# Optimization experiments

Hardware: AMD Instinct MI355X
Metric: run time of the kernel (lower is better)

The kernel has to match this reference:

```python
import jax, jax.numpy as jnp
import numpy as np

B, S, D, H, M = 4, 4096, 768, 12, 256
Dh = D // H
EPS_KERNEL = 1e-4
LN_EPS = 1e-5


def setup_inputs() -> dict:
    key = jax.random.key(0)
    ks = jax.random.split(key, 18)
    w = lambda k, sh: jax.random.normal(k, sh, jnp.float32) * 0.02
    return {
        "x": jax.random.normal(ks[0], (B, S, D), jnp.float32),
        # FAVOR+ random projection (performer uses orthogonal gaussian; gaussian here, same math)
        "proj": jax.random.normal(ks[1], (M, Dh), jnp.float32),
        "wq": w(ks[2], (D, D)), "bq": jnp.zeros((D,), jnp.float32),
        "wk": w(ks[3], (D, D)), "bk": jnp.zeros((D,), jnp.float32),
        "wv": w(ks[4], (D, D)), "bv": jnp.zeros((D,), jnp.float32),
        "wo": w(ks[5], (D, D)), "bo": jnp.zeros((D,), jnp.float32),
        "ln1_g": jnp.ones((D,), jnp.float32), "ln1_b": jnp.zeros((D,), jnp.float32),
        "ln2_g": jnp.ones((D,), jnp.float32), "ln2_b": jnp.zeros((D,), jnp.float32),
        "w1": w(ks[6], (4 * D, D)), "b1": jnp.zeros((4 * D,), jnp.float32),
        "w2": w(ks[7], (D, 4 * D)), "b2": jnp.zeros((D,), jnp.float32),
    }


def layernorm(x, g, b):
    mu = x.mean(-1, keepdims=True)
    var = ((x - mu) ** 2).mean(-1, keepdims=True)
    return (x - mu) / jnp.sqrt(var + LN_EPS) * g + b


def softmax_features(data, proj, is_query):
    # FAVOR+ positive softmax kernel features (performer-pytorch softmax_kernel)
    norm = data.shape[-1] ** -0.25
    ratio = proj.shape[0] ** -0.5
    dd = jnp.einsum('bhnd,md->bhnm', data * norm, proj)       # [B,H,S,M]
    diag = (data ** 2).sum(-1, keepdims=True) * 0.5 * norm * norm
    if is_query:
        mx = jnp.max(dd, axis=-1, keepdims=True)
    else:
        mx = jnp.max(dd)
    return ratio * (jnp.exp(dd - diag - mx) + EPS_KERNEL)


def performer_block(x, proj, wq, bq, wk, bk, wv, bv, wo, bo,
                    ln1_g, ln1_b, ln2_g, ln2_b, w1, b1, w2, b2):
    h = layernorm(x, ln1_g, ln1_b)
    split = lambda t: t.reshape(B, S, H, Dh).transpose(0, 2, 1, 3)  # [B,H,S,Dh]
    q = split(h @ wq.T + bq)
    k = split(h @ wk.T + bk)
    v = split(h @ wv.T + bv)

    qp = softmax_features(q, proj, True)    # [B,H,S,M]
    kp = softmax_features(k, proj, False)   # [B,H,S,M]

    # non-causal linear attention
    k_sum = kp.sum(axis=2)                                   # [B,H,M]
    d_inv = 1.0 / jnp.einsum('bhnm,bhm->bhn', qp, k_sum)     # [B,H,S]
    ctx = jnp.einsum('bhnm,bhnd->bhmd', kp, v)               # [B,H,M,Dh]
    attn = jnp.einsum('bhnm,bhmd,bhn->bhnd', qp, ctx, d_inv) # [B,H,S,Dh]
    attn = attn.transpose(0, 2, 1, 3).reshape(B, S, D)
    x = x + attn @ wo.T + bo

    h2 = layernorm(x, ln2_g, ln2_b)
    h2 = jax.nn.gelu(h2 @ w1.T + b1, approximate=False)
    x = x + h2 @ w2.T + b2
    return x


def reference(x, proj, wq, bq, wk, bk, wv, bv, wo, bo,
              ln1_g, ln1_b, ln2_g, ln2_b, w1, b1, w2, b2):
    return performer_block(x, proj, wq, bq, wk, bk, wv, bv, wo, bo,
                           ln1_g, ln1_b, ln2_g, ln2_b, w1, b1, w2, b2)
```

## Files before the change

### kernel.cpp

```cpp
#include <hip/hip_runtime.h>
#include <math.h>

typedef __attribute__((ext_vector_type(8))) short bf16x8;
typedef __attribute__((ext_vector_type(4))) float f32x4;

__device__ __forceinline__ float b2f(unsigned short u) {
    return __uint_as_float(((unsigned)u) << 16);
}
__device__ __forceinline__ unsigned short f2b(float f) {
    unsigned u = __float_as_uint(f);
    u += 0x7FFF + ((u >> 16) & 1);
    return (unsigned short)(u >> 16);
}
__device__ __forceinline__ void up2(unsigned u, float& a, float& b) {
    a = __uint_as_float(u << 16);
    b = __uint_as_float(u & 0xffff0000u);
}
__device__ __forceinline__ float gelu_exact(float v) {
    return 0.5f * v * (1.0f + erff(v * 0.70710678118654752f));
}
__device__ __forceinline__ void atomicMaxFloat(float* addr, float val) {
    unsigned* ua = (unsigned*)addr;
    unsigned old = *ua;
    while (true) {
        float of = __uint_as_float(old);
        if (of >= val) break;
        unsigned assumed = old;
        old = atomicCAS(ua, assumed, __float_as_uint(val));
        if (old == assumed) break;
    }
}
__device__ __forceinline__ void gl_lds16(const unsigned short* g, unsigned short* lds) {
    __builtin_amdgcn_global_load_lds((const __attribute__((address_space(1))) unsigned int*)g,
                                     (__attribute__((address_space(3))) unsigned int*)lds, 16, 0, 0);
}

__global__ __launch_bounds__(256)
void cvt_qkvp(const float* __restrict__ wq, const float* __restrict__ wk, const float* __restrict__ wv,
              const float* __restrict__ prj, unsigned short* __restrict__ wdst,
              unsigned short* __restrict__ pdst, float* __restrict__ ksum, float* __restrict__ kmax) {
    if (blockIdx.x < 48) {
        ksum[blockIdx.x * 256 + threadIdx.x] = 0.0f;
        if (blockIdx.x == 0 && threadIdx.x == 0) *kmax = -3.0e38f;
    }
    int i4 = (blockIdx.x * 256 + threadIdx.x) * 4;
    const float* s; unsigned short* d; int off;
    if (i4 < 1769472) { s = (i4 < 589824) ? wq : (i4 < 1179648 ? wk : wv);
        off = (i4 < 589824) ? i4 : (i4 < 1179648 ? i4 - 589824 : i4 - 1179648);
        d = wdst + i4; }
    else { s = prj; off = i4 - 1769472; d = pdst + off; }
    float4 v = *(const float4*)&s[off];
    ushort4 o; o.x = f2b(v.x); o.y = f2b(v.y); o.z = f2b(v.z); o.w = f2b(v.w);
    *(ushort4*)d = o;
}
__global__ __launch_bounds__(256)
void cvt_ow12(const float* __restrict__ wo, const float* __restrict__ w1, const float* __restrict__ w2,
              unsigned short* __restrict__ dst) {
    int i4 = (blockIdx.x * 256 + threadIdx.x) * 4;
    const float* s; int off;
    if (i4 < 589824) { s = wo; off = i4; }
    else if (i4 < 2949120) { s = w1; off = i4 - 589824; }
    else { s = w2; off = i4 - 2949120; }
    float4 v = *(const float4*)&s[off];
    ushort4 o; o.x = f2b(v.x); o.y = f2b(v.y); o.z = f2b(v.z); o.w = f2b(v.w);
    *(ushort4*)&dst[i4] = o;
}

template <bool IN_F32>
__global__ __launch_bounds__(256)
void ln_kernel(const void* __restrict__ Xv, const float* __restrict__ G,
               const float* __restrict__ Bb, unsigned short* __restrict__ OUT) {
    int row = blockIdx.x, t = threadIdx.x, wave = t >> 6, lane = t & 63;
    __shared__ float red[4];
    float x0, x1, x2;
    if constexpr (IN_F32) {
        const float* xr = (const float*)Xv + (size_t)row * 768;
        x0 = xr[t]; x1 = xr[t + 256]; x2 = xr[t + 512];
    } else {
        const unsigned short* xr = (const unsigned short*)Xv + (size_t)row * 768;
        x0 = b2f(xr[t]); x1 = b2f(xr[t + 256]); x2 = b2f(xr[t + 512]);
    }
    float s = x0 + x1 + x2;
#pragma unroll
    for (int d = 32; d; d >>= 1) s += __shfl_xor(s, d, 64);
    if (lane == 0) red[wave] = s;
    __syncthreads();
    float mean = (red[0] + red[1] + red[2] + red[3]) * (1.0f / 768.0f);
    __syncthreads();
    float d0 = x0 - mean, d1 = x1 - mean, d2 = x2 - mean;
    float s2 = d0 * d0 + d1 * d1 + d2 * d2;
#pragma unroll
    for (int d = 32; d; d >>= 1) s2 += __shfl_xor(s2, d, 64);
    if (lane == 0) red[wave] = s2;
    __syncthreads();
    float var = (red[0] + red[1] + red[2] + red[3]) * (1.0f / 768.0f);
    float inv = rsqrtf(var + 1e-5f);
    size_t base = (size_t)row * 768;
    OUT[base + t]       = f2b(d0 * inv * G[t]       + Bb[t]);
    OUT[base + t + 256] = f2b(d1 * inv * G[t + 256] + Bb[t + 256]);
    OUT[base + t + 512] = f2b(d2 * inv * G[t + 512] + Bb[t + 512]);
}

template <int EPI, bool R_F32, bool C_F32>
__global__ __launch_bounds__(512, 2)
void gemm_bt_256(const unsigned short* __restrict__ A, const unsigned short* __restrict__ Bm,
                 const float* __restrict__ bias, const void* __restrict__ R,
                 void* __restrict__ C, int N, int K, float alpha) {
    __shared__ unsigned short sA[2][256 * 64];
    __shared__ unsigned short sB[2][256 * 64];
    const int t = threadIdx.x;
    const int wave = t >> 6, lane = t & 63, quad = lane >> 4, l16 = lane & 15;
    const int nwg = gridDim.x * gridDim.y;
    int flat = blockIdx.y * gridDim.x + blockIdx.x;
    int q = nwg >> 3, r = nwg & 7;
    int xcd = flat & 7, idx = flat >> 3;
    int swz = (xcd < r ? xcd * (q + 1) : r * (q + 1) + (xcd - r) * q) + idx;
    const int m0 = (swz / gridDim.x) * 256;
    const int n0 = (swz % gridDim.x) * 256;
    const int wm = (wave >> 2) * 128, wn = (wave & 3) * 64;
    const int srow = t >> 3;
    const int scol = ((t & 7) ^ (srow & 7)) << 3;
    const unsigned short* gA = &A[(size_t)(m0 + srow) * K + scol];
    const unsigned short* gB = &Bm[(size_t)(n0 + srow) * K + scol];
    const size_t rstep = (size_t)64 * K;
    unsigned short* ldA0 = &sA[0][wave * 512];
    unsigned short* ldB0 = &sB[0][wave * 512];
    unsigned short* ldA1 = &sA[1][wave * 512];
    unsigned short* ldB1 = &sB[1][wave * 512];
    const int k0off = ((quad ^ (l16 & 7)) & 7) << 3;
    const int k1off = (((4 | quad) ^ (l16 & 7)) & 7) << 3;
    f32x4 acc[8][4] = {};
    const int nt = K >> 6;
#pragma unroll
    for (int u = 0; u < 4; ++u) {
        gl_lds16(gA + u * rstep, ldA0 + u * 4096);
        gl_lds16(gB + u * rstep, ldB0 + u * 4096);
    }
    __syncthreads();
    int cur = 0;
    for (int it = 0; it < nt; ++it) {
        if (it + 1 < nt) {
            const size_t kt = (size_t)(it + 1) << 6;
            unsigned short* dA = cur ? ldA0 : ldA1;
            unsigned short* dB = cur ? ldB0 : ldB1;
#pragma unroll
            for (int u = 0; u < 4; ++u) {
                gl_lds16(gA + u * rstep + kt, dA + u * 4096);
                gl_lds16(gB + u * rstep + kt, dB + u * 4096);
            }
        }
        const unsigned short* bufA = cur ? &sA[1][0] : &sA[0][0];
        const unsigned short* bufB = cur ? &sB[1][0] : &sB[0][0];
#pragma unroll
        for (int ks = 0; ks < 2; ++ks) {
            const int koff = ks ? k1off : k0off;
            bf16x8 bfr[4];
#pragma unroll
            for (int j = 0; j < 4; ++j)
                bfr[j] = *(const bf16x8*)&bufB[(wn + j * 16 + l16) * 64 + koff];
#pragma unroll
            for (int i = 0; i < 8; ++i) {
                bf16x8 af = *(const bf16x8*)&bufA[(wm + i * 16 + l16) * 64 + koff];
#pragma unroll
                for (int j = 0; j < 4; ++j)
                    acc[i][j] = __builtin_amdgcn_mfma_f32_16x16x32_bf16(af, bfr[j], acc[i][j], 0, 0, 0);
            }
        }
        __syncthreads();
        cur ^= 1;
    }
    if constexpr (EPI == 3) {
#pragma unroll
        for (int i = 0; i < 8; ++i) {
            int rowb = m0 + wm + i * 16 + quad * 4;
            int b_ = rowb >> 12, sbase = rowb & 4095;
#pragma unroll
            for (int j = 0; j < 4; ++j) {
                int col = n0 + wn + j * 16 + l16;
                float bs = bias[col];
                ushort4 o;
                o.x = f2b(acc[i][j][0] + bs);
                o.y = f2b(acc[i][j][1] + bs);
                o.z = f2b(acc[i][j][2] + bs);
                o.w = f2b(acc[i][j][3] + bs);
                size_t dst = (((size_t)b_ * 12 + (col >> 6)) * 64 + (col & 63)) * 4096 + sbase;
                *(ushort4*)&((unsigned short*)C)[dst] = o;
            }
        }
        return;
    }
#pragma unroll
    for (int i = 0; i < 8; ++i) {
        int rowb = m0 + wm + i * 16 + quad * 4;
#pragma unroll
        for (int j = 0; j < 4; ++j) {
            int col = n0 + wn + j * 16 + l16;
            float bs = bias[col];
#pragma unroll
            for (int r4 = 0; r4 < 4; ++r4) {
                size_t idx = (size_t)(rowb + r4) * N + col;
                float v = acc[i][j][r4] + bs;
                if constexpr (EPI == 0) v *= alpha;
                if constexpr (EPI == 1) {
                    if constexpr (R_F32) v += ((const float*)R)[idx];
                    else                 v += b2f(((const unsigned short*)R)[idx]);
                }
                if constexpr (EPI == 2) v = gelu_exact(v);
                if constexpr (C_F32) ((float*)C)[idx] = v;
                else                 ((unsigned short*)C)[idx] = f2b(v);
            }
        }
    }
}

__global__ __launch_bounds__(512, 2)
void gemm_qkv(const unsigned short* __restrict__ A, const unsigned short* __restrict__ Bm,
              const float* __restrict__ BQ, const float* __restrict__ BK,
              const float* __restrict__ BV, unsigned short* __restrict__ Cq,
              unsigned short* __restrict__ Ck, unsigned short* __restrict__ VT, float alpha) {
    const int K = 768;
    __shared__ unsigned short sA[2][256 * 64];
    __shared__ unsigned short sB[2][256 * 64];
    const int t = threadIdx.x;
    const int wave = t >> 6, lane = t & 63, quad = lane >> 4, l16 = lane & 15;
    const int nwg = gridDim.x * gridDim.y;
    int flat = blockIdx.y * gridDim.x + blockIdx.x;
    int q = nwg >> 3, r = nwg & 7;
    int xcd = flat & 7, idx = flat >> 3;
    int swz = (xcd < r ? xcd * (q + 1) : r * (q + 1) + (xcd - r) * q) + idx;
    const int m0 = (swz / gridDim.x) * 256;
    const int n0 = (swz % gridDim.x) * 256;
    const int wm = (wave >> 2) * 128, wn = (wave & 3) * 64;
    const int srow = t >> 3;
    const int scol = ((t & 7) ^ (srow & 7)) << 3;
    const unsigned short* gA = &A[(size_t)(m0 + srow) * K + scol];
    const unsigned short* gB = &Bm[(size_t)(n0 + srow) * K + scol];
    const size_t rstep = (size_t)64 * K;
    unsigned short* ldA0 = &sA[0][wave * 512];
    unsigned short* ldB0 = &sB[0][wave * 512];
    unsigned short* ldA1 = &sA[1][wave * 512];
    unsigned short* ldB1 = &sB[1][wave * 512];
    const int k0off = ((quad ^ (l16 & 7)) & 7) << 3;
    const int k1off = (((4 | quad) ^ (l16 & 7)) & 7) << 3;
    f32x4 acc[8][4] = {};
    const int nt = K >> 6;
#pragma unroll
    for (int u = 0; u < 4; ++u) {
        gl_lds16(gA + u * rstep, ldA0 + u * 4096);
        gl_lds16(gB + u * rstep, ldB0 + u * 4096);
    }
    __syncthreads();
    int cur = 0;
    for (int it = 0; it < nt; ++it) {
        if (it + 1 < nt) {
            const size_t kt = (size_t)(it + 1) << 6;
            unsigned short* dA = cur ? ldA0 : ldA1;
            unsigned short* dB = cur ? ldB0 : ldB1;
#pragma unroll
            for (int u = 0; u < 4; ++u) {
                gl_lds16(gA + u * rstep + kt, dA + u * 4096);
                gl_lds16(gB + u * rstep + kt, dB + u * 4096);
            }
        }
        const unsigned short* bufA = cur ? &sA[1][0] : &sA[0][0];
        const unsigned short* bufB = cur ? &sB[1][0] : &sB[0][0];
#pragma unroll
        for (int ks = 0; ks < 2; ++ks) {
            const int koff = ks ? k1off : k0off;
            bf16x8 bfr[4];
#pragma unroll
            for (int j = 0; j < 4; ++j)
                bfr[j] = *(const bf16x8*)&bufB[(wn + j * 16 + l16) * 64 + koff];
#pragma unroll
            for (int i = 0; i < 8; ++i) {
                bf16x8 af = *(const bf16x8*)&bufA[(wm + i * 16 + l16) * 64 + koff];
#pragma unroll
                for (int j = 0; j < 4; ++j)
                    acc[i][j] = __builtin_amdgcn_mfma_f32_16x16x32_bf16(af, bfr[j], acc[i][j], 0, 0, 0);
            }
        }
        __syncthreads();
        cur ^= 1;
    }
    const int seg = n0 / 768;
    const int nbase = n0 - seg * 768;
    const float* bias = (seg == 0) ? BQ : (seg == 1 ? BK : BV);
    if (seg == 2) {
#pragma unroll
        for (int i = 0; i < 8; ++i) {
            int rowb = m0 + wm + i * 16 + quad * 4;
            int b_ = rowb >> 12, sbase = rowb & 4095;
#pragma unroll
            for (int j = 0; j < 4; ++j) {
                int col = nbase + wn + j * 16 + l16;
                float bs = bias[col];
                ushort4 o;
                o.x = f2b(acc[i][j][0] + bs);
                o.y = f2b(acc[i][j][1] + bs);
                o.z = f2b(acc[i][j][2] + bs);
                o.w = f2b(acc[i][j][3] + bs);
                size_t dst = (((size_t)b_ * 12 + (col >> 6)) * 64 + (col & 63)) * 4096 + sbase;
                *(ushort4*)&VT[dst] = o;
            }
        }
    } else {
        unsigned short* Cn = (seg == 0) ? Cq : Ck;
#pragma unroll
        for (int i = 0; i < 8; ++i) {
            int rowb = m0 + wm + i * 16 + quad * 4;
#pragma unroll
            for (int j = 0; j < 4; ++j) {
                int col = nbase + wn + j * 16 + l16;
                float bs = bias[col];
#pragma unroll
                for (int r4 = 0; r4 < 4; ++r4) {
                    size_t idxo = (size_t)(rowb + r4) * 768 + col;
                    Cn[idxo] = f2b((acc[i][j][r4] + bs) * alpha);
                }
            }
        }
    }
}

template <int MODE>
__global__ __launch_bounds__(256)
void feat_kernel(const unsigned short* __restrict__ Q, const unsigned short* __restrict__ P,
                 unsigned short* __restrict__ OUTP, float* __restrict__ kmaxp,
                 float* __restrict__ ksump) {
    __shared__ unsigned short sQ[64 * 64];
    __shared__ unsigned short sP[256 * 64];
    __shared__ float sDiag[64];
    __shared__ float sRed[4];
    int t = threadIdx.x, wave = t >> 6, lane = t & 63, quad = lane >> 4, l16 = lane & 15;
    int bh = blockIdx.y, bq = bh / 12, hh = bh % 12;
    int s0 = blockIdx.x * 64;
    size_t rowbase = (size_t)bq * 4096 + s0;
#pragma unroll
    for (int u = 0; u < 2; ++u) {
        int L = u * 256 + t, row = L >> 3, c8 = (L & 7) * 8;
        *(uint4*)&sQ[row * 64 + c8] = *(const uint4*)&Q[(rowbase + row) * 768 + hh * 64 + c8];
    }
#pragma unroll
    for (int u = 0; u < 8; ++u) {
        int L = u * 256 + t, row = L >> 3, c8 = (L & 7) * 8;
        *(uint4*)&sP[row * 64 + c8] = *(const uint4*)&P[(size_t)row * 64 + c8];
    }
    __syncthreads();
    if (MODE != 1 && t < 64) {
        float d = 0.0f;
        for (int c = 0; c < 64; ++c) { float f = b2f(sQ[t * 64 + c]); d += f * f; }
        sDiag[t] = 0.5f * d;
    }
    f32x4 acc[4][4] = {};
#pragma unroll
    for (int ks = 0; ks < 2; ++ks) {
        bf16x8 af[4], bfr[4];
#pragma unroll
        for (int i = 0; i < 4; ++i) af[i] = *(const bf16x8*)&sQ[(i * 16 + l16) * 64 + ks * 32 + quad * 8];
#pragma unroll
        for (int j = 0; j < 4; ++j) bfr[j] = *(const bf16x8*)&sP[(wave * 64 + j * 16 + l16) * 64 + ks * 32 + quad * 8];
#pragma unroll
        for (int i = 0; i < 4; ++i)
#pragma unroll
            for (int j = 0; j < 4; ++j)
                acc[i][j] = __builtin_amdgcn_mfma_f32_16x16x32_bf16(af[i], bfr[j], acc[i][j], 0, 0, 0);
    }
    if constexpr (MODE == 1) {
        float m = -3.0e38f;
#pragma unroll
        for (int i = 0; i < 4; ++i)
#pragma unroll
            for (int j = 0; j < 4; ++j)
#pragma unroll
                for (int r = 0; r < 4; ++r) m = fmaxf(m, acc[i][j][r]);
#pragma unroll
        for (int d = 1; d < 64; d <<= 1) m = fmaxf(m, __shfl_xor(m, d, 64));
        if (lane == 0) sRed[wave] = m;
        __syncthreads();
        if (t == 0) atomicMaxFloat(kmaxp, fmaxf(fmaxf(sRed[0], sRed[1]), fmaxf(sRed[2], sRed[3])));
        return;
    } else {
        __syncthreads();
        float mx_k = *kmaxp;
        float csum[4] = {0.0f, 0.0f, 0.0f, 0.0f};
#pragma unroll
        for (int i = 0; i < 4; ++i)
#pragma unroll
            for (int j = 0; j < 4; ++j) {
                int col = wave * 64 + j * 16 + l16;
                ushort4 o;
#pragma unroll
                for (int r = 0; r < 4; ++r) {
                    int row = i * 16 + quad * 4 + r;
                    float v = 0.0625f * (expf(acc[i][j][r] - sDiag[row] - mx_k) + 1e-4f);
                    csum[j] += v;
                    (&o.x)[r] = f2b(v);
                }
                *(ushort4*)&OUTP[((size_t)bh * 256 + col) * 4096 + s0 + i * 16 + quad * 4] = o;
            }
#pragma unroll
        for (int j = 0; j < 4; ++j) {
            csum[j] += __shfl_xor(csum[j], 16, 64);
            csum[j] += __shfl_xor(csum[j], 32, 64);
        }
        if (quad == 0)
#pragma unroll
            for (int j = 0; j < 4; ++j)
                atomicAdd(&ksump[bh * 256 + wave * 64 + j * 16 + l16], csum[j]);
    }
}

__global__ __launch_bounds__(256)
void ctx_gemm(const unsigned short* __restrict__ KPT, const unsigned short* __restrict__ VT,
              float* __restrict__ part) {
    __shared__ unsigned short sV[2][64 * 32];
    __shared__ unsigned short sK[2][128 * 32];
    const int t = threadIdx.x;
    const int wave = t >> 6, lane = t & 63, quad = lane >> 4, l16 = lane & 15;
    const int bh = blockIdx.y;
    const int sc = blockIdx.x >> 1, mh = blockIdx.x & 1;
    const int m0 = mh * 128;
    const int k0 = sc * 512;
    const int srow = t >> 2;
    const int scol = ((t & 3) ^ (srow & 3)) << 3;
    const unsigned short* gv  = &VT [((size_t)bh * 64 + srow) * 4096 + k0 + scol];
    const unsigned short* gk0 = &KPT[((size_t)bh * 256 + m0 + srow) * 4096 + k0 + scol];
    const unsigned short* gk1 = &KPT[((size_t)bh * 256 + m0 + 64 + srow) * 4096 + k0 + scol];
    const int ldsoff = wave * 512;
    const int sw = ((quad ^ l16) & 3) << 3;
    f32x4 acc[4][2] = {};
    gl_lds16(gv,  &sV[0][ldsoff]);
    gl_lds16(gk0, &sK[0][ldsoff]);
    gl_lds16(gk1, &sK[0][2048 + ldsoff]);
    __syncthreads();
    int cur = 0;
    for (int it = 0; it < 16; ++it) {
        if (it + 1 < 16) {
            const int kt = (it + 1) << 5;
            gl_lds16(gv + kt,  &sV[cur ^ 1][ldsoff]);
            gl_lds16(gk0 + kt, &sK[cur ^ 1][ldsoff]);
            gl_lds16(gk1 + kt, &sK[cur ^ 1][2048 + ldsoff]);
        }
        bf16x8 af[4], bfr[2];
#pragma unroll
        for (int i = 0; i < 4; ++i) af[i] = *(const bf16x8*)&sV[cur][(i * 16 + l16) * 32 + sw];
#pragma unroll
        for (int j = 0; j < 2; ++j) bfr[j] = *(const bf16x8*)&sK[cur][(wave * 32 + j * 16 + l16) * 32 + sw];
#pragma unroll
        for (int i = 0; i < 4; ++i)
#pragma unroll
            for (int j = 0; j < 2; ++j)
                acc[i][j] = __builtin_amdgcn_mfma_f32_16x16x32_bf16(af[i], bfr[j], acc[i][j], 0, 0, 0);
        __syncthreads();
        cur ^= 1;
    }
    float* base = part + ((size_t)(sc * 48 + bh) * 64) * 256;
#pragma unroll
    for (int i = 0; i < 4; ++i)
#pragma unroll
        for (int r = 0; r < 4; ++r) {
            int d = i * 16 + quad * 4 + r;
#pragma unroll
            for (int j = 0; j < 2; ++j) {
                int m = m0 + wave * 32 + j * 16 + l16;
                base[(size_t)d * 256 + m] = acc[i][j][r];
            }
        }
}

__global__ __launch_bounds__(256)
void ctx_reduce(const float* __restrict__ part, unsigned short* __restrict__ ctxb) {
    size_t i = (size_t)blockIdx.x * 256 + threadIdx.x;
    float s = 0.0f;
#pragma unroll
    for (int c = 0; c < 8; ++c) s += part[(size_t)c * 786432 + i];
    ctxb[i] = f2b(s);
}

__global__ __launch_bounds__(256)
void feat_attn(const unsigned short* __restrict__ Q, const unsigned short* __restrict__ P,
               const unsigned short* __restrict__ CTX, const float* __restrict__ ksump,
               unsigned short* __restrict__ ATT) {
    __shared__ unsigned short sQ[64 * 64];
    __shared__ unsigned short sPQ[256 * 64];
    __shared__ unsigned short sCtx[64 * 256];
    __shared__ float sDiag[64];
    __shared__ float sRed[256];
    __shared__ float sWred[256];
    __shared__ float sKs[256];
    __shared__ float sDinv[64];
    int t = threadIdx.x, wave = t >> 6, lane = t & 63, quad = lane >> 4, l16 = lane & 15;
    int bh = blockIdx.y, bq = bh / 12, hh = bh % 12;
    int s0 = blockIdx.x * 64;
    size_t rowbase = (size_t)bq * 4096 + s0;
#pragma unroll
    for (int u = 0; u < 2; ++u) {
        int L = u * 256 + t, row = L >> 3, c8 = (L & 7) * 8;
        *(uint4*)&sQ[row * 64 + c8] = *(const uint4*)&Q[(rowbase + row) * 768 + hh * 64 + c8];
    }
#pragma unroll
    for (int u = 0; u < 8; ++u) {
        int L = u * 256 + t, row = L >> 3, c8 = (L & 7) * 8;
        *(uint4*)&sPQ[row * 64 + c8] = *(const uint4*)&P[(size_t)row * 64 + c8];
    }
#pragma unroll
    for (int u = 0; u < 8; ++u) {
        int L = u * 256 + t, d = L >> 5, m8 = L & 31;
        int m8s = (m8 & 28) | ((m8 ^ d) & 3);
        *(uint4*)&sCtx[d * 256 + m8s * 8] = *(const uint4*)&CTX[(size_t)bh * 16384 + d * 256 + m8 * 8];
    }
    sKs[t] = ksump[bh * 256 + t];
    __syncthreads();
    if (t < 64) {
        float d = 0.0f;
        for (int c = 0; c < 64; ++c) { float f = b2f(sQ[t * 64 + c]); d += f * f; }
        sDiag[t] = 0.5f * d;
    }
    f32x4 acc[4][4] = {};
#pragma unroll
    for (int ks = 0; ks < 2; ++ks) {
        bf16x8 af[4], bfr[4];
#pragma unroll
        for (int i = 0; i < 4; ++i) af[i] = *(const bf16x8*)&sQ[(i * 16 + l16) * 64 + ks * 32 + quad * 8];
#pragma unroll
        for (int j = 0; j < 4; ++j) bfr[j] = *(const bf16x8*)&sPQ[(wave * 64 + j * 16 + l16) * 64 + ks * 32 + quad * 8];
#pragma unroll
        for (int i = 0; i < 4; ++i)
#pragma unroll
            for (int j = 0; j < 4; ++j)
                acc[i][j] = __builtin_amdgcn_mfma_f32_16x16x32_bf16(af[i], bfr[j], acc[i][j], 0, 0, 0);
    }
#pragma unroll
    for (int i = 0; i < 4; ++i)
#pragma unroll
        for (int r = 0; r < 4; ++r) {
            float m = fmaxf(fmaxf(acc[i][0][r], acc[i][1][r]), fmaxf(acc[i][2][r], acc[i][3][r]));
#pragma unroll
            for (int d = 1; d < 16; d <<= 1) m = fmaxf(m, __shfl_xor(m, d, 64));
            if (l16 == 0) sRed[wave * 64 + i * 16 + quad * 4 + r] = m;
        }
    __syncthreads();
    if (t < 64) sRed[t] = fmaxf(fmaxf(sRed[t], sRed[64 + t]), fmaxf(sRed[128 + t], sRed[192 + t]));
    __syncthreads();
#pragma unroll
    for (int i = 0; i < 4; ++i)
#pragma unroll
        for (int r = 0; r < 4; ++r) {
            int row = i * 16 + quad * 4 + r;
            float diag = sDiag[row], mx = sRed[row];
            float p = 0.0f;
#pragma unroll
            for (int j = 0; j < 4; ++j) {
                int col = wave * 64 + j * 16 + l16;
                float v = 0.0625f * (expf(acc[i][j][r] - diag - mx) + 1e-4f);
                int colp = (col & ~31) | ((((col >> 3) ^ row) & 3) << 3) | (col & 7);
                sPQ[row * 256 + colp] = f2b(v);
                p += v * sKs[col];
            }
#pragma unroll
            for (int d = 1; d < 16; d <<= 1) p += __shfl_xor(p, d, 64);
            if (l16 == 0) sWred[wave * 64 + row] = p;
        }
    __syncthreads();
    if (t < 64) sDinv[t] = 1.0f / (sWred[t] + sWred[64 + t] + sWred[128 + t] + sWred[192 + t]);
    __syncthreads();
    const int w16 = wave * 16;
    const int aswz = ((quad ^ (l16 & 3)) << 3);
    f32x4 acc2[4] = {};
    const unsigned short* qrow = &sPQ[(w16 + l16) * 256];
#pragma unroll
    for (int kt = 0; kt < 256; kt += 32) {
        bf16x8 af = *(const bf16x8*)&qrow[kt + aswz];
#pragma unroll
        for (int j = 0; j < 4; ++j) {
            bf16x8 bf = *(const bf16x8*)&sCtx[(j * 16 + l16) * 256 + kt + aswz];
            acc2[j] = __builtin_amdgcn_mfma_f32_16x16x32_bf16(af, bf, acc2[j], 0, 0, 0);
        }
    }
#pragma unroll
    for (int rr = 0; rr < 4; ++rr) {
        int sr = w16 + quad * 4 + rr;
        float dv = sDinv[sr];
        size_t obase = ((size_t)bq * 4096 + s0 + sr) * 768 + hh * 64;
#pragma unroll
        for (int j = 0; j < 4; ++j)
            ATT[obase + j * 16 + l16] = f2b(acc2[j][rr] * dv);
    }
}

extern "C" void kernel_launch(void* const* d_in, const int* in_sizes, int n_in,
                              void* d_out, int out_size, void* d_ws, size_t ws_size,
                              hipStream_t stream) {
    const float* X   = (const float*)d_in[0];
    const float* PRJ = (const float*)d_in[1];
    const float* WQ  = (const float*)d_in[2];
    const float* BQ  = (const float*)d_in[3];
    const float* WK  = (const float*)d_in[4];
    const float* BKb = (const float*)d_in[5];
    const float* WV  = (const float*)d_in[6];
    const float* BV  = (const float*)d_in[7];
    const float* WO  = (const float*)d_in[8];
    const float* BO  = (const float*)d_in[9];
    const float* G1  = (const float*)d_in[10];
    const float* Bn1 = (const float*)d_in[11];
    const float* G2  = (const float*)d_in[12];
    const float* Bn2 = (const float*)d_in[13];
    const float* W1  = (const float*)d_in[14];
    const float* Bf1 = (const float*)d_in[15];
    const float* W2  = (const float*)d_in[16];
    const float* Bf2 = (const float*)d_in[17];
    float* OUT = (float*)d_out;

    char* w = (char*)d_ws;
    const size_t SZ_ACT = (size_t)16384 * 768 * 2;
    unsigned short* hbuf  = (unsigned short*)(w);
    float*          part  = (float*)(w);
    unsigned short* qn    = (unsigned short*)(w + SZ_ACT);
    unsigned short* wow12 = (unsigned short*)(w + SZ_ACT);
    unsigned short* kn    = (unsigned short*)(w + 2 * SZ_ACT);
    unsigned short* x2    = (unsigned short*)(w + 2 * SZ_ACT);
    unsigned short* vtb   = (unsigned short*)(w + 3 * SZ_ACT);
    unsigned short* attn  = (unsigned short*)(w + 3 * SZ_ACT);
    unsigned short* wqkv  = (unsigned short*)(w + 4 * SZ_ACT);
    unsigned short* kpt   = (unsigned short*)(w + 4 * SZ_ACT);
    unsigned short* gmid  = kpt;
    char* tail = w + 4 * SZ_ACT + (size_t)100663296;
    unsigned short* prjb = (unsigned short*)(tail);
    unsigned short* ctxb = (unsigned short*)(tail + 32768);
    float* ksum = (float*)(tail + 32768 + 1572864);
    float* kmax = (float*)(tail + 32768 + 1572864 + 49152);

    unsigned short* w1b = wow12 + 589824;
    unsigned short* w2b = wow12 + 2949120;
    unsigned short* wob = wow12;

    const float NORM = 0.35355339059327373f;

    cvt_qkvp<<<1744, 256, 0, stream>>>(WQ, WK, WV, PRJ, wqkv, prjb, ksum, kmax);
    ln_kernel<true><<<16384, 256, 0, stream>>>(X, G1, Bn1, hbuf);
    gemm_qkv<<<dim3(9, 64), 512, 0, stream>>>(hbuf, wqkv, BQ, BKb, BV, qn, kn, vtb, NORM);
    feat_kernel<1><<<dim3(64, 48), 256, 0, stream>>>(kn, prjb, nullptr, kmax, ksum);
    feat_kernel<2><<<dim3(64, 48), 256, 0, stream>>>(kn, prjb, kpt, kmax, ksum);
    ctx_gemm<<<dim3(16, 48), 256, 0, stream>>>(kpt, vtb, part);
    ctx_reduce<<<3072, 256, 0, stream>>>(part, ctxb);
    feat_attn<<<dim3(64, 48), 256, 0, stream>>>(qn, prjb, ctxb, ksum, attn);
    cvt_ow12<<<5184, 256, 0, stream>>>(WO, W1, W2, wow12);
    gemm_bt_256<1, true, false><<<dim3(3, 64), 512, 0, stream>>>(attn, wob, BO, X, x2, 768, 768, 1.0f);
    ln_kernel<false><<<16384, 256, 0, stream>>>(x2, G2, Bn2, hbuf);
    gemm_bt_256<2, false, false><<<dim3(12, 64), 512, 0, stream>>>(hbuf, w1b, Bf1, nullptr, gmid, 3072, 768, 1.0f);
    gemm_bt_256<1, false, true><<<dim3(3, 64), 512, 0, stream>>>(gmid, w2b, Bf2, x2, OUT, 768, 3072, 1.0f);
}
```

Before: 685.4 us.

## Add phased-pipeline GEMM with XCD swizzle for the FFN up-projection

Adds a new bf16 MFMA GEMM kernel for the W1+GELU GEMM. It splits each K-tile into four compute phases and interleaves the global-to-LDS loads for the next tiles between them, using explicit vmcnt waits and raw barriers instead of __syncthreads. It also remaps workgroups across XCDs for cache locality and raises wave priority around the MFMA bursts. The goal is better overlap of memory loads with compute in the largest GEMM, at the cost of fragile hand-tuned wait counts and higher register pressure.

Result: slower. 703.5 us (+2.7%).

```diff
diff --git a/kernel.cpp b/kernel.cpp
--- a/kernel.cpp
+++ b/kernel.cpp
@@ -33,6 +33,12 @@
 __device__ __forceinline__ void gl_lds16(const unsigned short* g, unsigned short* lds) {
     __builtin_amdgcn_global_load_lds((const __attribute__((address_space(1))) unsigned int*)g,
                                      (__attribute__((address_space(3))) unsigned int*)lds, 16, 0, 0);
+}
+template <int N> __device__ __forceinline__ void wait_vm() {
+    if constexpr (N == 0) asm volatile("s_waitcnt vmcnt(0)" ::: "memory");
+    if constexpr (N == 4) asm volatile("s_waitcnt vmcnt(4)" ::: "memory");
+    if constexpr (N == 6) asm volatile("s_waitcnt vmcnt(6)" ::: "memory");
+    if constexpr (N == 8) asm volatile("s_waitcnt vmcnt(8)" ::: "memory");
 }
 
 __global__ __launch_bounds__(256)
@@ -168,6 +174,131 @@
         }
         __syncthreads();
         cur ^= 1;
+    }
+    if constexpr (EPI == 3) {
+#pragma unroll
+        for (int i = 0; i < 8; ++i) {
+            int rowb = m0 + wm + i * 16 + quad * 4;
+            int b_ = rowb >> 12, sbase = rowb & 4095;
+#pragma unroll
+            for (int j = 0; j < 4; ++j) {
+                int col = n0 + wn + j * 16 + l16;
+                float bs = bias[col];
+                ushort4 o;
+                o.x = f2b(acc[i][j][0] + bs);
+                o.y = f2b(acc[i][j][1] + bs);
+                o.z = f2b(acc[i][j][2] + bs);
+                o.w = f2b(acc[i][j][3] + bs);
+                size_t dst = (((size_t)b_ * 12 + (col >> 6)) * 64 + (col & 63)) * 4096 + sbase;
+                *(ushort4*)&((unsigned short*)C)[dst] = o;
+            }
+        }
+        return;
+    }
+#pragma unroll
+    for (int i = 0; i < 8; ++i) {
+        int rowb = m0 + wm + i * 16 + quad * 4;
+#pragma unroll
+        for (int j = 0; j < 4; ++j) {
+            int col = n0 + wn + j * 16 + l16;
+            float bs = bias[col];
+#pragma unroll
+            for (int r4 = 0; r4 < 4; ++r4) {
+                size_t idx = (size_t)(rowb + r4) * N + col;
+                float v = acc[i][j][r4] + bs;
+                if constexpr (EPI == 0) v *= alpha;
+                if constexpr (EPI == 1) {
+                    if constexpr (R_F32) v += ((const float*)R)[idx];
+                    else                 v += b2f(((const unsigned short*)R)[idx]);
+                }
+                if constexpr (EPI == 2) v = gelu_exact(v);
+                if constexpr (C_F32) ((float*)C)[idx] = v;
+                else                 ((unsigned short*)C)[idx] = f2b(v);
+            }
+        }
+    }
+}
+
+template <int EPI, bool R_F32, bool C_F32>
+__global__ __launch_bounds__(512, 2)
+void gemm_8ph(const unsigned short* __restrict__ A, const unsigned short* __restrict__ Bm,
+              const float* __restrict__ bias, const void* __restrict__ R,
+              void* __restrict__ C, int N, int K, float alpha) {
+    __shared__ unsigned short sA[2][256 * 64];
+    __shared__ unsigned short sB[2][256 * 64];
+    const int t = threadIdx.x;
+    const int wave = t >> 6, lane = t & 63, quad = lane >> 4, l16 = lane & 15;
+    const int nwg = gridDim.x * gridDim.y;
+    int flat = blockIdx.y * gridDim.x + blockIdx.x;
+    int q = nwg >> 3, r = nwg & 7;
+    int xcd = flat & 7, idx = flat >> 3;
+    int swz = (xcd < r ? xcd * (q + 1) : r * (q + 1) + (xcd - r) * q) + idx;
+    const int m0 = (swz / gridDim.x) * 256;
+    const int n0 = (swz % gridDim.x) * 256;
+    const int wm = (wave >> 2) * 128, wn = (wave & 3) * 64;
+    const int aw = (wave >> 2) * 64;
+    const int bw = (wave & 3) * 32;
+    const int srow = t >> 3;
+    const int scol = ((t & 7) ^ (srow & 7)) << 3;
+    const int k0off = ((quad ^ (l16 & 7)) & 7) << 3;
+    const int k1off = (((4 | quad) ^ (l16 & 7)) & 7) << 3;
+    const int brow = ((t >> 3) & 31);
+    const int bg   = (t >> 8);
+    f32x4 acc[8][4] = {};
+    const int NT = K >> 6;
+    auto STAGE_A = [&](int tile, int h) {
+        unsigned short* d = &sA[tile & 1][h * 8192 + wave * 512];
+        const size_t kb = (size_t)tile << 6;
+        gl_lds16(&A[(size_t)(m0 + h * 64 + srow) * K + kb + scol], d);
+        gl_lds16(&A[(size_t)(m0 + 128 + h * 64 + srow) * K + kb + scol], d + 4096);
+    };
+    auto STAGE_B = [&](int tile, int j) {
+        unsigned short* d = &sB[tile & 1][j * 8192 + wave * 512];
+        const size_t kb = (size_t)tile << 6;
+        gl_lds16(&Bm[(size_t)(n0 + (0 + bg) * 64 + j * 32 + brow) * K + kb + scol], d);
+        gl_lds16(&Bm[(size_t)(n0 + (2 + bg) * 64 + j * 32 + brow) * K + kb + scol], d + 4096);
+    };
+    STAGE_A(0, 0); STAGE_B(0, 0); STAGE_A(0, 1); STAGE_B(0, 1);
+    STAGE_A(1, 0); STAGE_B(1, 0);
+    wait_vm<8>();
+    __builtin_amdgcn_s_barrier();
+    for (int kt = 0; kt < NT; ++kt) {
+        const unsigned short* bA = sA[kt & 1];
+        const unsigned short* bB = sB[kt & 1];
+        const bool s1 = (kt + 1 < NT), s2 = (kt + 2 < NT);
+#pragma unroll
+        for (int p = 0; p < 4; ++p) {
+            const int qi = p >> 1, qj = p & 1;
+            bf16x8 afr[4][2], bfr[2][2];
+#pragma unroll
+            for (int ii = 0; ii < 4; ++ii)
+#pragma unroll
+                for (int ks = 0; ks < 2; ++ks)
+                    afr[ii][ks] = *(const bf16x8*)&bA[(qi * 128 + aw + ii * 16 + l16) * 64 + (ks ? k1off : k0off)];
+#pragma unroll
+            for (int jj = 0; jj < 2; ++jj)
+#pragma unroll
+                for (int ks = 0; ks < 2; ++ks)
+                    bfr[jj][ks] = *(const bf16x8*)&bB[(qj * 128 + bw + jj * 16 + l16) * 64 + (ks ? k1off : k0off)];
+            if (p == 0 && s1) STAGE_A(kt + 1, 1);
+            if (p == 1 && s1) STAGE_B(kt + 1, 1);
+            if (p == 2 && s2) STAGE_A(kt + 2, 0);
+            if (p == 3 && s2) STAGE_B(kt + 2, 0);
+            __builtin_amdgcn_s_barrier();
+            __builtin_amdgcn_s_setprio(1);
+#pragma unroll
+            for (int ii = 0; ii < 4; ++ii)
+#pragma unroll
+                for (int jj = 0; jj < 2; ++jj)
+#pragma unroll
+                    for (int ks = 0; ks < 2; ++ks)
+                        acc[qi * 4 + ii][qj * 2 + jj] = __builtin_amdgcn_mfma_f32_16x16x32_bf16(
+                            afr[ii][ks], bfr[jj][ks], acc[qi * 4 + ii][qj * 2 + jj], 0, 0, 0);
+            __builtin_amdgcn_s_setprio(0);
+            if (p == 0) { if (s1) wait_vm<6>(); else wait_vm<0>(); }
+            if (p == 3 && s1) { if (s2) wait_vm<8>(); else wait_vm<4>(); }
+            __builtin_amdgcn_s_barrier();
+        }
     }
     if constexpr (EPI == 3) {
 #pragma unroll
@@ -647,6 +778,6 @@
     cvt_ow12<<<5184, 256, 0, stream>>>(WO, W1, W2, wow12);
     gemm_bt_256<1, true, false><<<dim3(3, 64), 512, 0, stream>>>(attn, wob, BO, X, x2, 768, 768, 1.0f);
     ln_kernel<false><<<16384, 256, 0, stream>>>(x2, G2, Bn2, hbuf);
-    gemm_bt_256<2, false, false><<<dim3(12, 64), 512, 0, stream>>>(hbuf, w1b, Bf1, nullptr, gmid, 3072, 768, 1.0f);
+    gemm_8ph<2, false, false><<<dim3(12, 64), 512, 0, stream>>>(hbuf, w1b, Bf1, nullptr, gmid, 3072, 768, 1.0f);
     gemm_bt_256<1, false, true><<<dim3(3, 64), 512, 0, stream>>>(gmid, w2b, Bf2, x2, OUT, 768, 3072, 1.0f);
 }
```
